# Optimization experiments

Measured on AMD Instinct MI355X. Metric: run time of the kernel, lower is better.

The kernel has to match this reference:

```python
import jax, jax.numpy as jnp
import numpy as np

NEG_INF = -1e18  # fp32 masking constant used by the original module


def setup_inputs() -> dict:
    key0 = jax.random.key(0)
    kq, kk, kv, km, ke = jax.random.split(key0, 5)
    B, L, H, C = 2, 2048, 16, 64
    query = jax.random.normal(kq, (B, L, H, C), dtype=jnp.float32)
    key = jax.random.normal(kk, (B, L, H, C), dtype=jnp.float32)
    value = jax.random.normal(kv, (B, L, H, C), dtype=jnp.float32)
    mask = jax.random.randint(km, (B, L, L), 0, 2).astype(jnp.bool_)
    edge_scores = jax.random.normal(ke, (1, H, L, L), dtype=jnp.float32)
    return {"query": query, "key": key, "value": value, "mask": mask,
            "edge_scores": edge_scores}


def _masked_softmax(att_score, mask):
    # mask: True -> keep, False -> masked. Fill with -1e18 (fp32 path),
    # softmax, then multiply by mask (post-softmax zeroing), as in original.
    s = jnp.where(mask, att_score, NEG_INF)
    w = jax.nn.softmax(s, axis=-1)
    return w * mask.astype(w.dtype)


def reference(query, key, value, mask, edge_scores):
    # layout 'NTK': query/key/value (B, L, H, C); mask (B, Lq, Lm)
    scale = jnp.sqrt(jnp.asarray(query.shape[-1], dtype=query.dtype))
    # scores: (B, H, Lq, Lm)
    scores = jnp.einsum('binc,bjnc->bnij', query, key)
    scores = scores + edge_scores
    attn_weights = _masked_softmax(scores / scale, mask[:, None, :, :])
    # dropout rate is 0.0 -> identity
    # context: (B, Lq, H, Cv) -> (B, Lq, H*Cv)
    context = jnp.einsum('bnij,bjnc->binc', attn_weights, value)
    B, Lq = context.shape[0], context.shape[1]
    context_vec = context.reshape(B, Lq, -1)
    return (context_vec, scores, attn_weights)
```

## Files before the change

### kernel.cpp

```cpp
#include <hip/hip_runtime.h>


typedef __attribute__((ext_vector_type(8))) short bf16x8;
typedef __attribute__((ext_vector_type(4))) float f32x4;

#define LQ 2048
#define NH 16
#define CD 64

__device__ inline short f2bf(float x) {
    union { float f; unsigned u; } v; v.f = x;
    unsigned r = v.u + 0x7FFFu + ((v.u >> 16) & 1u);
    return (short)(r >> 16);
}

__device__ inline bf16x8 pack8(float4 a, float4 b) {
    bf16x8 r;
    r[0] = f2bf(a.x); r[1] = f2bf(a.y); r[2] = f2bf(a.z); r[3] = f2bf(a.w);
    r[4] = f2bf(b.x); r[5] = f2bf(b.y); r[6] = f2bf(b.z); r[7] = f2bf(b.w);
    return r;
}

__global__ __launch_bounds__(256, 4)
void k_stats(const float* __restrict__ q, const float* __restrict__ kk,
             const float* __restrict__ edge, const int* __restrict__ mask,
             float* __restrict__ lsum)
{
    __shared__ short Ks[64][72];
    const int z = blockIdx.y;
    const int b = z & 1, h = z >> 1;
    const int i0 = blockIdx.x * 64;
    const int tid = threadIdx.x;
    const int r = tid >> 2, seg = (tid & 3) * 16;
    const int wave = tid >> 6, lane = tid & 63;
    const int quad = lane >> 4, mm = lane & 15;

    const int gi = i0 + wave * 16 + mm;
    const float* qp = q + ((size_t)((b * LQ + gi) * NH + h)) * CD;
    bf16x8 qa0 = pack8(*(const float4*)(qp + quad * 8), *(const float4*)(qp + quad * 8 + 4));
    bf16x8 qa1 = pack8(*(const float4*)(qp + 32 + quad * 8), *(const float4*)(qp + 32 + quad * 8 + 4));

    const float* erow = edge + ((size_t)(h * LQ + gi)) * LQ;
    const int*   mrow = mask + ((size_t)(b * LQ + gi)) * LQ;

    float4 ev[4]; int4 mv[4];
    #pragma unroll
    for (int jt = 0; jt < 4; ++jt) {
        ev[jt] = *(const float4*)(erow + jt * 16 + quad * 4);
        mv[jt] = *(const int4*)(mrow + jt * 16 + quad * 4);
    }

    float lacc = 0.f;

    for (int jb = 0; jb < 32; ++jb) {
        const int j0 = jb * 64;
        __syncthreads();
        const float* krow = kk + ((size_t)((b * LQ + j0 + r) * NH + h)) * CD + seg;
        #pragma unroll
        for (int u = 0; u < 4; ++u) {
            float4 g = ((const float4*)krow)[u];
            *(short4*)&Ks[r][seg + u * 4] = make_short4(f2bf(g.x), f2bf(g.y), f2bf(g.z), f2bf(g.w));
        }
        __syncthreads();

        f32x4 acc[4];
        #pragma unroll
        for (int jt = 0; jt < 4; ++jt) {
            bf16x8 k0 = *(const bf16x8*)&Ks[jt * 16 + mm][quad * 8];
            bf16x8 k1 = *(const bf16x8*)&Ks[jt * 16 + mm][32 + quad * 8];
            f32x4 a = {0.f, 0.f, 0.f, 0.f};
            a = __builtin_amdgcn_mfma_f32_16x16x32_bf16(k0, qa0, a, 0, 0, 0);
            a = __builtin_amdgcn_mfma_f32_16x16x32_bf16(k1, qa1, a, 0, 0, 0);
            acc[jt] = a;
        }

        #pragma unroll
        for (int jt = 0; jt < 4; ++jt) {
            float p0 = mv[jt].x ? __expf((acc[jt][0] + ev[jt].x) * 0.125f) : 0.f;
            float p1 = mv[jt].y ? __expf((acc[jt][1] + ev[jt].y) * 0.125f) : 0.f;
            float p2 = mv[jt].z ? __expf((acc[jt][2] + ev[jt].z) * 0.125f) : 0.f;
            float p3 = mv[jt].w ? __expf((acc[jt][3] + ev[jt].w) * 0.125f) : 0.f;
            lacc += (p0 + p1) + (p2 + p3);
        }

        if (jb < 31) {
            #pragma unroll
            for (int jt = 0; jt < 4; ++jt) {
                ev[jt] = *(const float4*)(erow + j0 + 64 + jt * 16 + quad * 4);
                mv[jt] = *(const int4*)(mrow + j0 + 64 + jt * 16 + quad * 4);
            }
        }
    }

    lacc += __shfl_xor(lacc, 16, 64);
    lacc += __shfl_xor(lacc, 32, 64);
    if (quad == 0)
        lsum[(size_t)(b * NH + h) * LQ + gi] = lacc;
}

__global__ __launch_bounds__(256, 4)
void k_fused(const float* __restrict__ q, const float* __restrict__ kk,
             const float* __restrict__ v, const int* __restrict__ mask,
             const float* __restrict__ edge, const float* __restrict__ lsum,
             float* __restrict__ sc, float* __restrict__ attn,
             float* __restrict__ ctx)
{
    __shared__ short Ks[64][72];
    __shared__ short Vt[64][72];
    __shared__ short Wt[4][16][72];

    const int z = blockIdx.y;
    const int b = z & 1, h = z >> 1;
    const int i0 = blockIdx.x * 64;
    const int tid = threadIdx.x;
    const int r = tid >> 2, seg = (tid & 3) * 16;
    const int wave = tid >> 6, lane = tid & 63;
    const int quad = lane >> 4, mm = lane & 15;

    const int gi = i0 + wave * 16 + mm;
    const float* qp = q + ((size_t)((b * LQ + gi) * NH + h)) * CD;
    bf16x8 qa0 = pack8(*(const float4*)(qp + quad * 8), *(const float4*)(qp + quad * 8 + 4));
    bf16x8 qa1 = pack8(*(const float4*)(qp + 32 + quad * 8), *(const float4*)(qp + 32 + quad * 8 + 4));

    const float* erow = edge + ((size_t)(h * LQ + gi)) * LQ;
    const int*   mrow = mask + ((size_t)(b * LQ + gi)) * LQ;
    const size_t srow = ((size_t)((b * NH + h) * LQ + gi)) * LQ;

    const float l = lsum[(size_t)(b * NH + h) * LQ + gi];
    const float inv = (l > 0.f) ? 1.f / l : 0.f;

    float4 ev[4]; int4 mv[4];
    #pragma unroll
    for (int jt = 0; jt < 4; ++jt) {
        ev[jt] = *(const float4*)(erow + jt * 16 + quad * 4);
        mv[jt] = *(const int4*)(mrow + jt * 16 + quad * 4);
    }

    f32x4 cacc[4] = { {0,0,0,0}, {0,0,0,0}, {0,0,0,0}, {0,0,0,0} };

    for (int jb = 0; jb < 32; ++jb) {
        const int j0 = jb * 64;
        __syncthreads();
        const float* krow = kk + ((size_t)((b * LQ + j0 + r) * NH + h)) * CD + seg;
        const float* vrow = v  + ((size_t)((b * LQ + j0 + r) * NH + h)) * CD + seg;
        #pragma unroll
        for (int u = 0; u < 4; ++u) {
            float4 g = ((const float4*)krow)[u];
            *(short4*)&Ks[r][seg + u * 4] = make_short4(f2bf(g.x), f2bf(g.y), f2bf(g.z), f2bf(g.w));
            float4 w = ((const float4*)vrow)[u];
            Vt[seg + u * 4 + 0][r] = f2bf(w.x);
            Vt[seg + u * 4 + 1][r] = f2bf(w.y);
            Vt[seg + u * 4 + 2][r] = f2bf(w.z);
            Vt[seg + u * 4 + 3][r] = f2bf(w.w);
        }
        __syncthreads();

        f32x4 acc[4];
        #pragma unroll
        for (int jt = 0; jt < 4; ++jt) {
            bf16x8 k0 = *(const bf16x8*)&Ks[jt * 16 + mm][quad * 8];
            bf16x8 k1 = *(const bf16x8*)&Ks[jt * 16 + mm][32 + quad * 8];
            f32x4 a = {0.f, 0.f, 0.f, 0.f};
            a = __builtin_amdgcn_mfma_f32_16x16x32_bf16(k0, qa0, a, 0, 0, 0);
            a = __builtin_amdgcn_mfma_f32_16x16x32_bf16(k1, qa1, a, 0, 0, 0);
            acc[jt] = a;
        }

        #pragma unroll
        for (int jt = 0; jt < 4; ++jt) {
            const int jl = jt * 16 + quad * 4;
            float4 s4 = make_float4(acc[jt][0] + ev[jt].x, acc[jt][1] + ev[jt].y,
                                    acc[jt][2] + ev[jt].z, acc[jt][3] + ev[jt].w);
            *(float4*)(sc + srow + j0 + jl) = s4;
            float w0 = mv[jt].x ? __expf(s4.x * 0.125f) * inv : 0.f;
            float w1 = mv[jt].y ? __expf(s4.y * 0.125f) * inv : 0.f;
            float w2 = mv[jt].z ? __expf(s4.z * 0.125f) * inv : 0.f;
            float w3 = mv[jt].w ? __expf(s4.w * 0.125f) * inv : 0.f;
            *(float4*)(attn + srow + j0 + jl) = make_float4(w0, w1, w2, w3);
            *(short4*)&Wt[wave][mm][jl] = make_short4(f2bf(w0), f2bf(w1), f2bf(w2), f2bf(w3));
        }

        if (jb < 31) {
            #pragma unroll
            for (int jt = 0; jt < 4; ++jt) {
                ev[jt] = *(const float4*)(erow + j0 + 64 + jt * 16 + quad * 4);
                mv[jt] = *(const int4*)(mrow + j0 + 64 + jt * 16 + quad * 4);
            }
        }

        #pragma unroll
        for (int kt = 0; kt < 2; ++kt) {
            bf16x8 aw = *(const bf16x8*)&Wt[wave][mm][kt * 32 + quad * 8];
            #pragma unroll
            for (int nt = 0; nt < 4; ++nt) {
                bf16x8 bb = *(const bf16x8*)&Vt[nt * 16 + mm][kt * 32 + quad * 8];
                cacc[nt] = __builtin_amdgcn_mfma_f32_16x16x32_bf16(aw, bb, cacc[nt], 0, 0, 0);
            }
        }
    }

    const int irow = i0 + wave * 16 + quad * 4;
    #pragma unroll
    for (int nt = 0; nt < 4; ++nt) {
        const int c = nt * 16 + mm;
        #pragma unroll
        for (int reg = 0; reg < 4; ++reg) {
            const int i = irow + reg;
            ctx[((size_t)(b * LQ + i)) * (NH * CD) + h * CD + c] = cacc[nt][reg];
        }
    }
}

extern "C" void kernel_launch(void* const* d_in, const int* in_sizes, int n_in,
                              void* d_out, int out_size, void* d_ws, size_t ws_size,
                              hipStream_t stream) {
    const float* q    = (const float*)d_in[0];
    const float* k    = (const float*)d_in[1];
    const float* v    = (const float*)d_in[2];
    const int*   mask = (const int*)d_in[3];
    const float* edge = (const float*)d_in[4];

    float* out = (float*)d_out;
    float* ctx = out;
    float* sc  = out + 4194304;
    float* at  = sc + 134217728;

    float* lsum = (float*)d_ws;

    k_stats<<<dim3(32, 32), 256, 0, stream>>>(q, k, edge, mask, lsum);
    k_fused<<<dim3(32, 32), 256, 0, stream>>>(q, k, v, mask, edge, lsum, sc, at, ctx);
}
```

Baseline: 1.653 ms.

## Drop stats pass via deferred softmax normalization and separate attn rescale kernel

The separate row-sum kernel is removed. The main kernel accumulates the softmax denominator while it writes unnormalized exp weights and scores, then scales the context rows by the inverse sum at the end. A new elementwise kernel rescales the stored attention matrix using the saved inverse sums. The change also prefetches K/V tiles into registers one iteration ahead, uses nontemporal loads and stores for the streaming edge/scores/attn traffic, and lowers the launch-bounds occupancy hint. This trades a second read of edge and mask for an extra read-modify-write pass over the large attention output.

Result: slower. 1.718 ms (+3.9%).

```diff
diff --git a/kernel.cpp b/kernel.cpp
--- a/kernel.cpp
+++ b/kernel.cpp
@@ -3,6 +3,7 @@
 
 typedef __attribute__((ext_vector_type(8))) short bf16x8;
 typedef __attribute__((ext_vector_type(4))) float f32x4;
+typedef __attribute__((ext_vector_type(4))) int   i32x4;
 
 #define LQ 2048
 #define NH 16
@@ -14,96 +15,19 @@
     return (short)(r >> 16);
 }
 
-__device__ inline bf16x8 pack8(float4 a, float4 b) {
+__device__ inline bf16x8 pack8(f32x4 a, f32x4 b) {
     bf16x8 r;
-    r[0] = f2bf(a.x); r[1] = f2bf(a.y); r[2] = f2bf(a.z); r[3] = f2bf(a.w);
-    r[4] = f2bf(b.x); r[5] = f2bf(b.y); r[6] = f2bf(b.z); r[7] = f2bf(b.w);
+    r[0] = f2bf(a[0]); r[1] = f2bf(a[1]); r[2] = f2bf(a[2]); r[3] = f2bf(a[3]);
+    r[4] = f2bf(b[0]); r[5] = f2bf(b[1]); r[6] = f2bf(b[2]); r[7] = f2bf(b[3]);
     return r;
 }
 
-__global__ __launch_bounds__(256, 4)
-void k_stats(const float* __restrict__ q, const float* __restrict__ kk,
-             const float* __restrict__ edge, const int* __restrict__ mask,
-             float* __restrict__ lsum)
-{
-    __shared__ short Ks[64][72];
-    const int z = blockIdx.y;
-    const int b = z & 1, h = z >> 1;
-    const int i0 = blockIdx.x * 64;
-    const int tid = threadIdx.x;
-    const int r = tid >> 2, seg = (tid & 3) * 16;
-    const int wave = tid >> 6, lane = tid & 63;
-    const int quad = lane >> 4, mm = lane & 15;
-
-    const int gi = i0 + wave * 16 + mm;
-    const float* qp = q + ((size_t)((b * LQ + gi) * NH + h)) * CD;
-    bf16x8 qa0 = pack8(*(const float4*)(qp + quad * 8), *(const float4*)(qp + quad * 8 + 4));
-    bf16x8 qa1 = pack8(*(const float4*)(qp + 32 + quad * 8), *(const float4*)(qp + 32 + quad * 8 + 4));
-
-    const float* erow = edge + ((size_t)(h * LQ + gi)) * LQ;
-    const int*   mrow = mask + ((size_t)(b * LQ + gi)) * LQ;
-
-    float4 ev[4]; int4 mv[4];
-    #pragma unroll
-    for (int jt = 0; jt < 4; ++jt) {
-        ev[jt] = *(const float4*)(erow + jt * 16 + quad * 4);
-        mv[jt] = *(const int4*)(mrow + jt * 16 + quad * 4);
-    }
-
-    float lacc = 0.f;
-
-    for (int jb = 0; jb < 32; ++jb) {
-        const int j0 = jb * 64;
-        __syncthreads();
-        const float* krow = kk + ((size_t)((b * LQ + j0 + r) * NH + h)) * CD + seg;
-        #pragma unroll
-        for (int u = 0; u < 4; ++u) {
-            float4 g = ((const float4*)krow)[u];
-            *(short4*)&Ks[r][seg + u * 4] = make_short4(f2bf(g.x), f2bf(g.y), f2bf(g.z), f2bf(g.w));
-        }
-        __syncthreads();
-
-        f32x4 acc[4];
-        #pragma unroll
-        for (int jt = 0; jt < 4; ++jt) {
-            bf16x8 k0 = *(const bf16x8*)&Ks[jt * 16 + mm][quad * 8];
-            bf16x8 k1 = *(const bf16x8*)&Ks[jt * 16 + mm][32 + quad * 8];
-            f32x4 a = {0.f, 0.f, 0.f, 0.f};
-            a = __builtin_amdgcn_mfma_f32_16x16x32_bf16(k0, qa0, a, 0, 0, 0);
-            a = __builtin_amdgcn_mfma_f32_16x16x32_bf16(k1, qa1, a, 0, 0, 0);
-            acc[jt] = a;
-        }
-
-        #pragma unroll
-        for (int jt = 0; jt < 4; ++jt) {
-            float p0 = mv[jt].x ? __expf((acc[jt][0] + ev[jt].x) * 0.125f) : 0.f;
-            float p1 = mv[jt].y ? __expf((acc[jt][1] + ev[jt].y) * 0.125f) : 0.f;
-            float p2 = mv[jt].z ? __expf((acc[jt][2] + ev[jt].z) * 0.125f) : 0.f;
-            float p3 = mv[jt].w ? __expf((acc[jt][3] + ev[jt].w) * 0.125f) : 0.f;
-            lacc += (p0 + p1) + (p2 + p3);
-        }
-
-        if (jb < 31) {
-            #pragma unroll
-            for (int jt = 0; jt < 4; ++jt) {
-                ev[jt] = *(const float4*)(erow + j0 + 64 + jt * 16 + quad * 4);
-                mv[jt] = *(const int4*)(mrow + j0 + 64 + jt * 16 + quad * 4);
-            }
-        }
-    }
-
-    lacc += __shfl_xor(lacc, 16, 64);
-    lacc += __shfl_xor(lacc, 32, 64);
-    if (quad == 0)
-        lsum[(size_t)(b * NH + h) * LQ + gi] = lacc;
-}
-
-__global__ __launch_bounds__(256, 4)
-void k_fused(const float* __restrict__ q, const float* __restrict__ kk,
-             const float* __restrict__ v, const int* __restrict__ mask,
-             const float* __restrict__ edge, const float* __restrict__ lsum,
-             float* __restrict__ sc, float* __restrict__ attn,
-             float* __restrict__ ctx)
+__global__ __launch_bounds__(256, 3)
+void k_main(const float* __restrict__ q, const float* __restrict__ kk,
+            const float* __restrict__ v, const int* __restrict__ mask,
+            const float* __restrict__ edge,
+            float* __restrict__ sc, float* __restrict__ attn,
+            float* __restrict__ ctx, float* __restrict__ invout)
 {
     __shared__ short Ks[64][72];
     __shared__ short Vt[64][72];
@@ -119,39 +43,47 @@
 
     const int gi = i0 + wave * 16 + mm;
     const float* qp = q + ((size_t)((b * LQ + gi) * NH + h)) * CD;
-    bf16x8 qa0 = pack8(*(const float4*)(qp + quad * 8), *(const float4*)(qp + quad * 8 + 4));
-    bf16x8 qa1 = pack8(*(const float4*)(qp + 32 + quad * 8), *(const float4*)(qp + 32 + quad * 8 + 4));
+    bf16x8 qa0 = pack8(*(const f32x4*)(qp + quad * 8), *(const f32x4*)(qp + quad * 8 + 4));
+    bf16x8 qa1 = pack8(*(const f32x4*)(qp + 32 + quad * 8), *(const f32x4*)(qp + 32 + quad * 8 + 4));
 
     const float* erow = edge + ((size_t)(h * LQ + gi)) * LQ;
     const int*   mrow = mask + ((size_t)(b * LQ + gi)) * LQ;
     const size_t srow = ((size_t)((b * NH + h) * LQ + gi)) * LQ;
 
-    const float l = lsum[(size_t)(b * NH + h) * LQ + gi];
-    const float inv = (l > 0.f) ? 1.f / l : 0.f;
-
-    float4 ev[4]; int4 mv[4];
+    f32x4 ev[4]; i32x4 mv[4];
     #pragma unroll
     for (int jt = 0; jt < 4; ++jt) {
-        ev[jt] = *(const float4*)(erow + jt * 16 + quad * 4);
-        mv[jt] = *(const int4*)(mrow + jt * 16 + quad * 4);
+        ev[jt] = __builtin_nontemporal_load((const f32x4*)(erow + jt * 16 + quad * 4));
+        mv[jt] = *(const i32x4*)(mrow + jt * 16 + quad * 4);
+    }
+    f32x4 kr[4], vr[4];
+    {
+        const float* kp = kk + ((size_t)((b * LQ + r) * NH + h)) * CD + seg;
+        const float* vp = v  + ((size_t)((b * LQ + r) * NH + h)) * CD + seg;
+        #pragma unroll
+        for (int u = 0; u < 4; ++u) { kr[u] = ((const f32x4*)kp)[u]; vr[u] = ((const f32x4*)vp)[u]; }
     }
 
+    float lacc = 0.f;
     f32x4 cacc[4] = { {0,0,0,0}, {0,0,0,0}, {0,0,0,0}, {0,0,0,0} };
 
     for (int jb = 0; jb < 32; ++jb) {
         const int j0 = jb * 64;
         __syncthreads();
-        const float* krow = kk + ((size_t)((b * LQ + j0 + r) * NH + h)) * CD + seg;
-        const float* vrow = v  + ((size_t)((b * LQ + j0 + r) * NH + h)) * CD + seg;
         #pragma unroll
         for (int u = 0; u < 4; ++u) {
-            float4 g = ((const float4*)krow)[u];
-            *(short4*)&Ks[r][seg + u * 4] = make_short4(f2bf(g.x), f2bf(g.y), f2bf(g.z), f2bf(g.w));
-            float4 w = ((const float4*)vrow)[u];
-            Vt[seg + u * 4 + 0][r] = f2bf(w.x);
-            Vt[seg + u * 4 + 1][r] = f2bf(w.y);
-            Vt[seg + u * 4 + 2][r] = f2bf(w.z);
-            Vt[seg + u * 4 + 3][r] = f2bf(w.w);
+            *(short4*)&Ks[r][seg + u * 4] =
+                make_short4(f2bf(kr[u][0]), f2bf(kr[u][1]), f2bf(kr[u][2]), f2bf(kr[u][3]));
+            Vt[seg + u * 4 + 0][r] = f2bf(vr[u][0]);
+            Vt[seg + u * 4 + 1][r] = f2bf(vr[u][1]);
+            Vt[seg + u * 4 + 2][r] = f2bf(vr[u][2]);
+            Vt[seg + u * 4 + 3][r] = f2bf(vr[u][3]);
+        }
+        if (jb < 31) {
+            const float* kp = kk + ((size_t)((b * LQ + j0 + 64 + r) * NH + h)) * CD + seg;
+            const float* vp = v  + ((size_t)((b * LQ + j0 + 64 + r) * NH + h)) * CD + seg;
+            #pragma unroll
+            for (int u = 0; u < 4; ++u) { kr[u] = ((const f32x4*)kp)[u]; vr[u] = ((const f32x4*)vp)[u]; }
         }
         __syncthreads();
 
@@ -169,22 +101,23 @@
         #pragma unroll
         for (int jt = 0; jt < 4; ++jt) {
             const int jl = jt * 16 + quad * 4;
-            float4 s4 = make_float4(acc[jt][0] + ev[jt].x, acc[jt][1] + ev[jt].y,
-                                    acc[jt][2] + ev[jt].z, acc[jt][3] + ev[jt].w);
-            *(float4*)(sc + srow + j0 + jl) = s4;
-            float w0 = mv[jt].x ? __expf(s4.x * 0.125f) * inv : 0.f;
-            float w1 = mv[jt].y ? __expf(s4.y * 0.125f) * inv : 0.f;
-            float w2 = mv[jt].z ? __expf(s4.z * 0.125f) * inv : 0.f;
-            float w3 = mv[jt].w ? __expf(s4.w * 0.125f) * inv : 0.f;
-            *(float4*)(attn + srow + j0 + jl) = make_float4(w0, w1, w2, w3);
-            *(short4*)&Wt[wave][mm][jl] = make_short4(f2bf(w0), f2bf(w1), f2bf(w2), f2bf(w3));
+            f32x4 s4 = acc[jt] + ev[jt];
+            __builtin_nontemporal_store(s4, (f32x4*)(sc + srow + j0 + jl));
+            f32x4 p;
+            p[0] = mv[jt][0] ? __expf(s4[0] * 0.125f) : 0.f;
+            p[1] = mv[jt][1] ? __expf(s4[1] * 0.125f) : 0.f;
+            p[2] = mv[jt][2] ? __expf(s4[2] * 0.125f) : 0.f;
+            p[3] = mv[jt][3] ? __expf(s4[3] * 0.125f) : 0.f;
+            __builtin_nontemporal_store(p, (f32x4*)(attn + srow + j0 + jl));
+            *(short4*)&Wt[wave][mm][jl] = make_short4(f2bf(p[0]), f2bf(p[1]), f2bf(p[2]), f2bf(p[3]));
+            lacc += (p[0] + p[1]) + (p[2] + p[3]);
         }
 
         if (jb < 31) {
             #pragma unroll
             for (int jt = 0; jt < 4; ++jt) {
-                ev[jt] = *(const float4*)(erow + j0 + 64 + jt * 16 + quad * 4);
-                mv[jt] = *(const int4*)(mrow + j0 + 64 + jt * 16 + quad * 4);
+                ev[jt] = __builtin_nontemporal_load((const f32x4*)(erow + j0 + 64 + jt * 16 + quad * 4));
+                mv[jt] = *(const i32x4*)(mrow + j0 + 64 + jt * 16 + quad * 4);
             }
         }
 
@@ -199,6 +132,17 @@
         }
     }
 
+    lacc += __shfl_xor(lacc, 16, 64);
+    lacc += __shfl_xor(lacc, 32, 64);
+    const float inv = (lacc > 0.f) ? 1.f / lacc : 0.f;
+    if (quad == 0)
+        invout[(size_t)(b * NH + h) * LQ + gi] = inv;
+
+    float inv4[4];
+    #pragma unroll
+    for (int reg = 0; reg < 4; ++reg)
+        inv4[reg] = __shfl(inv, quad * 4 + reg, 64);
+
     const int irow = i0 + wave * 16 + quad * 4;
     #pragma unroll
     for (int nt = 0; nt < 4; ++nt) {
@@ -206,8 +150,23 @@
         #pragma unroll
         for (int reg = 0; reg < 4; ++reg) {
             const int i = irow + reg;
-            ctx[((size_t)(b * LQ + i)) * (NH * CD) + h * CD + c] = cacc[nt][reg];
+            __builtin_nontemporal_store(cacc[nt][reg] * inv4[reg],
+                                        ctx + ((size_t)(b * LQ + i)) * (NH * CD) + h * CD + c);
         }
+    }
+}
+
+__global__ __launch_bounds__(256)
+void k_norm(float* __restrict__ attn, const float* __restrict__ inv)
+{
+    const size_t total4 = (size_t)2 * NH * LQ * LQ / 4;
+    size_t idx = (size_t)blockIdx.x * 256 + threadIdx.x;
+    const size_t stride = (size_t)gridDim.x * 256;
+    for (; idx < total4; idx += stride) {
+        const float iv = inv[(idx * 4) >> 11];
+        f32x4 w = __builtin_nontemporal_load((const f32x4*)attn + idx);
+        w *= iv;
+        __builtin_nontemporal_store(w, (f32x4*)attn + idx);
     }
 }
 
@@ -225,8 +184,8 @@
     float* sc  = out + 4194304;
     float* at  = sc + 134217728;
 
-    float* lsum = (float*)d_ws;
+    float* inv = (float*)d_ws;
 
-    k_stats<<<dim3(32, 32), 256, 0, stream>>>(q, k, edge, mask, lsum);
-    k_fused<<<dim3(32, 32), 256, 0, stream>>>(q, k, v, mask, edge, lsum, sc, at, ctx);
+    k_main<<<dim3(32, 32), 256, 0, stream>>>(q, k, v, mask, edge, sc, at, ctx, inv);
+    k_norm<<<dim3(2048), 256, 0, stream>>>(at, inv);
 }
```
